# Optimization experiments

Measured on AMD Instinct MI355X. Metric: run time of the kernel, lower is better.

Reference implementation:

```python
import jax, jax.numpy as jnp
import numpy as np

SEQ, BATCH, D_MODEL, N_HEADS = 2048, 2, 1024, 16
HEAD_DIM = D_MODEL // N_HEADS


def setup_inputs() -> dict:
    key = jax.random.key(0)
    ks = jax.random.split(key, 5)
    scale = 1.0 / np.sqrt(D_MODEL)
    x = jax.random.normal(ks[0], (SEQ, BATCH, D_MODEL), dtype=jnp.float32)
    Wq = jax.random.normal(ks[1], (D_MODEL, D_MODEL), dtype=jnp.float32) * scale
    Wk = jax.random.normal(ks[2], (D_MODEL, D_MODEL), dtype=jnp.float32) * scale
    Wv = jax.random.normal(ks[3], (D_MODEL, D_MODEL), dtype=jnp.float32) * scale
    Wo = jax.random.normal(ks[4], (D_MODEL, D_MODEL), dtype=jnp.float32) * scale
    return {"x": x, "Wq": Wq, "Wk": Wk, "Wv": Wv, "Wo": Wo}


def reference(x, Wq, Wk, Wv, Wo):
    # x: (S, B, D). torch nn.Linear(bias=False): y = x @ W.T with W (out,in)
    S, B, D = x.shape
    H, Hd = N_HEADS, HEAD_DIM
    q = (x @ Wq.T).reshape(S, B, H, Hd)
    k = (x @ Wk.T).reshape(S, B, H, Hd)
    v = (x @ Wv.T).reshape(S, B, H, Hd)
    # scores: (B, H, S, S)
    scores = jnp.einsum("sbhd,tbhd->bhst", q, k) / jnp.sqrt(jnp.float32(Hd))
    causal = jnp.triu(jnp.ones((S, S), dtype=bool), k=1)  # True above diagonal
    scores = jnp.where(causal[None, None, :, :], -jnp.inf, scores)
    probs = jax.nn.softmax(scores, axis=-1)
    # out: (S, B, H, Hd) -> (S, B, D)
    attn = jnp.einsum("bhst,tbhd->sbhd", probs, v).reshape(S, B, D)
    return attn @ Wo.T
```

## Files before the change

### kernel.cpp

```cpp
#include <hip/hip_runtime.h>
#include <math.h>

#define SEQ     2048
#define BATCH   2
#define DMODEL  1024
#define NHEADS  16
#define HDIM    64
#define MROWS   (SEQ * BATCH)
#define KDIM    1024

typedef _Float16 half8  __attribute__((ext_vector_type(8)));
typedef _Float16 half2v __attribute__((ext_vector_type(2)));
typedef float    f32x4  __attribute__((ext_vector_type(4)));

__device__ inline void gload_lds16(const void* g, void* lds_uniform) {
    __builtin_amdgcn_global_load_lds(
        (const __attribute__((address_space(1))) void*)g,
        (__attribute__((address_space(3))) void*)lds_uniform,
        16, 0, 0);
}

__global__ __launch_bounds__(256)
void cvt_f32_f16(const float* __restrict__ s, _Float16* __restrict__ d, int n8) {
    const int i = blockIdx.x * 256 + threadIdx.x;
    if (i < n8) {
        const float4* sp = reinterpret_cast<const float4*>(s) + (size_t)i * 2;
        const float4 x0 = sp[0], x1 = sp[1];
        const half8 h = {(_Float16)x0.x, (_Float16)x0.y, (_Float16)x0.z, (_Float16)x0.w,
                         (_Float16)x1.x, (_Float16)x1.y, (_Float16)x1.z, (_Float16)x1.w};
        *(reinterpret_cast<half8*>(d) + i) = h;
    }
}

#define GBM 128
#define GBN 64

template<int AMODE, int QKV>
__global__ __launch_bounds__(256)
void gemm_k(const void* __restrict__ Ap, const _Float16* __restrict__ Wall,
            void* __restrict__ C0, void* __restrict__ C1, void* __restrict__ C2)
{
    __shared__ _Float16 As[2][GBM * 32];
    __shared__ _Float16 Bs[2][GBN * 32];

    const int tid  = threadIdx.x;
    const int wid  = tid >> 6;
    const int lane = tid & 63;
    const int m0 = blockIdx.y * GBM;
    const int n0 = blockIdx.x * GBN;
    const int wr = (wid >> 1) * 64;
    const int wc = (wid & 1) * 32;

    const _Float16* Wh = QKV ? (Wall + (size_t)blockIdx.z * KDIM * DMODEL) : Wall;

    const int a_row = tid >> 2;
    const int a_col = (tid & 3) * 8;
    const int b_row = wid * 16 + (lane >> 2);
    const int b_col = (lane & 3) * 8;

    const float*    Af0 = (const float*)Ap    + (size_t)(m0 + a_row)      * KDIM + a_col;
    const float*    Af1 = (const float*)Ap    + (size_t)(m0 + a_row + 64) * KDIM + a_col;
    const _Float16* Ah0 = (const _Float16*)Ap + (size_t)(m0 + a_row)      * KDIM + a_col;
    const _Float16* Ah1 = (const _Float16*)Ap + (size_t)(m0 + a_row + 64) * KDIM + a_col;
    const _Float16* Wr  = Wh + (size_t)(n0 + b_row) * KDIM + b_col;

    const int frow = lane & 15;
    const int kb   = (lane >> 4) * 8;

    f32x4 acc[4][2] = {};

    for (int k0 = 0; k0 < KDIM; k0 += 64) {
        #pragma unroll
        for (int s = 0; s < 2; ++s) {
            const int kk = k0 + s * 32;
            gload_lds16(Wr + kk, (char*)Bs[s] + wid * 1024);
            if constexpr (AMODE == 0) {
                const float4 a0 = *reinterpret_cast<const float4*>(Af0 + kk);
                const float4 a1 = *reinterpret_cast<const float4*>(Af0 + kk + 4);
                const float4 a2 = *reinterpret_cast<const float4*>(Af1 + kk);
                const float4 a3 = *reinterpret_cast<const float4*>(Af1 + kk + 4);
                const half8 h0 = {(_Float16)a0.x, (_Float16)a0.y, (_Float16)a0.z, (_Float16)a0.w,
                                  (_Float16)a1.x, (_Float16)a1.y, (_Float16)a1.z, (_Float16)a1.w};
                const half8 h1 = {(_Float16)a2.x, (_Float16)a2.y, (_Float16)a2.z, (_Float16)a2.w,
                                  (_Float16)a3.x, (_Float16)a3.y, (_Float16)a3.z, (_Float16)a3.w};
                *reinterpret_cast<half8*>((char*)As[s] + tid * 16)        = h0;
                *reinterpret_cast<half8*>((char*)As[s] + 4096 + tid * 16) = h1;
            } else {
                *reinterpret_cast<half8*>((char*)As[s] + tid * 16) =
                    *reinterpret_cast<const half8*>(Ah0 + kk);
                *reinterpret_cast<half8*>((char*)As[s] + 4096 + tid * 16) =
                    *reinterpret_cast<const half8*>(Ah1 + kk);
            }
        }
        __syncthreads();

        #pragma unroll
        for (int s = 0; s < 2; ++s) {
            half8 af[4], bf[2];
            #pragma unroll
            for (int fm = 0; fm < 4; ++fm)
                af[fm] = *reinterpret_cast<const half8*>(&As[s][(wr + fm * 16 + frow) * 32 + kb]);
            #pragma unroll
            for (int fn = 0; fn < 2; ++fn)
                bf[fn] = *reinterpret_cast<const half8*>(&Bs[s][(wc + fn * 16 + frow) * 32 + kb]);
            #pragma unroll
            for (int fm = 0; fm < 4; ++fm)
                #pragma unroll
                for (int fn = 0; fn < 2; ++fn)
                    acc[fm][fn] = __builtin_amdgcn_mfma_f32_16x16x32_f16(
                        af[fm], bf[fn], acc[fm][fn], 0, 0, 0);
        }
        __syncthreads();
    }

    const int crow = (lane >> 4) * 4;
    const int ccol = lane & 15;
    if constexpr (QKV == 0) {
        float* C = (float*)C0;
        #pragma unroll
        for (int fm = 0; fm < 4; ++fm)
            #pragma unroll
            for (int fn = 0; fn < 2; ++fn)
                #pragma unroll
                for (int r = 0; r < 4; ++r)
                    C[(size_t)(m0 + wr + fm * 16 + crow + r) * DMODEL
                      + n0 + wc + fn * 16 + ccol] = acc[fm][fn][r];
    } else {
        if (blockIdx.z < 2) {
            _Float16* C = (_Float16*)(blockIdx.z == 0 ? C0 : C1);
            #pragma unroll
            for (int fm = 0; fm < 4; ++fm)
                #pragma unroll
                for (int fn = 0; fn < 2; ++fn)
                    #pragma unroll
                    for (int r = 0; r < 4; ++r)
                        C[(size_t)(m0 + wr + fm * 16 + crow + r) * DMODEL
                          + n0 + wc + fn * 16 + ccol] = (_Float16)acc[fm][fn][r];
        } else {
            _Float16* Vt = (_Float16*)C2;
            const int hh = blockIdx.x;
            #pragma unroll
            for (int fm = 0; fm < 4; ++fm)
                #pragma unroll
                for (int fn = 0; fn < 2; ++fn) {
                    const int d  = wc + fn * 16 + ccol;
                    const int s0 = (m0 + wr + fm * 16 + crow) >> 1;
                    const half2v lo = {(_Float16)acc[fm][fn][0], (_Float16)acc[fm][fn][2]};
                    const half2v hi = {(_Float16)acc[fm][fn][1], (_Float16)acc[fm][fn][3]};
                    *reinterpret_cast<half2v*>(Vt + ((size_t)(hh * 64 + d)) * SEQ + s0) = lo;
                    *reinterpret_cast<half2v*>(Vt + ((size_t)((16 + hh) * 64 + d)) * SEQ + s0) = hi;
                }
        }
    }
}

__global__ __launch_bounds__(256)
void attn_mfma(const _Float16* __restrict__ Qh, const _Float16* __restrict__ Kh,
               const _Float16* __restrict__ Vt, _Float16* __restrict__ Ab)
{
    __shared__ _Float16 Qs[64 * 64];
    __shared__ _Float16 Ks[64 * 64];
    __shared__ _Float16 Vs[64 * 64];
    __shared__ _Float16 Ps[4 * 16 * 72];

    const int tid  = threadIdx.x;
    const int wid  = tid >> 6;
    const int lane = tid & 63;
    const int l4 = lane & 15, lg = lane >> 4;
    const int bh = blockIdx.y, b = bh >> 4, h = bh & 15;

    for (int half = 0; half < 2; ++half) {
        const int qt = half ? (31 - (int)blockIdx.x) : (int)blockIdx.x;
        const int q0 = qt * 64;

        __syncthreads();
        #pragma unroll
        for (int i = 0; i < 2; ++i) {
            const int row = i * 32 + wid * 8 + (lane >> 3);
            const int c   = (lane & 7) ^ (row & 7);
            gload_lds16(Qh + ((size_t)((q0 + row) * 2 + b)) * DMODEL + h * 64 + c * 8,
                        (char*)Qs + i * 4096 + wid * 1024);
        }
        __syncthreads();

        half8 qf[2];
        {
            const int row = wid * 16 + l4;
            #pragma unroll
            for (int ks = 0; ks < 2; ++ks) {
                const int p = (ks * 4 + lg) ^ (row & 7);
                qf[ks] = *reinterpret_cast<const half8*>((char*)Qs + row * 128 + p * 16);
            }
        }

        float m_r[4], l_r[4];
        f32x4 o[4] = {};
        #pragma unroll
        for (int r = 0; r < 4; ++r) { m_r[r] = -1e30f; l_r[r] = 0.f; }

        _Float16* Pw = Ps + wid * 16 * 72;
        const int ktiles = qt + 1;

        for (int kt = 0; kt < ktiles; ++kt) {
            const int t0 = kt * 64;
            __syncthreads();
            #pragma unroll
            for (int i = 0; i < 2; ++i) {
                const int row = i * 32 + wid * 8 + (lane >> 3);
                const int c   = (lane & 7) ^ (row & 7);
                gload_lds16(Kh + ((size_t)((t0 + row) * 2 + b)) * DMODEL + h * 64 + c * 8,
                            (char*)Ks + i * 4096 + wid * 1024);
                gload_lds16(Vt + ((size_t)(bh * 64 + row)) * SEQ + t0 + c * 8,
                            (char*)Vs + i * 4096 + wid * 1024);
            }
            __syncthreads();

            f32x4 sacc[4] = {};
            #pragma unroll
            for (int ks = 0; ks < 2; ++ks)
                #pragma unroll
                for (int fn = 0; fn < 4; ++fn) {
                    const int row = fn * 16 + l4;
                    const int p   = (ks * 4 + lg) ^ (row & 7);
                    const half8 bf = *reinterpret_cast<const half8*>((char*)Ks + row * 128 + p * 16);
                    sacc[fn] = __builtin_amdgcn_mfma_f32_16x16x32_f16(qf[ks], bf, sacc[fn], 0, 0, 0);
                }

            const int qbase = q0 + wid * 16 + lg * 4;
            float sv[4][4];
            #pragma unroll
            for (int fn = 0; fn < 4; ++fn) {
                const int tg = t0 + fn * 16 + l4;
                #pragma unroll
                for (int r = 0; r < 4; ++r)
                    sv[fn][r] = (tg <= qbase + r) ? sacc[fn][r] * 0.125f : -1e30f;
            }
            #pragma unroll
            for (int r = 0; r < 4; ++r) {
                float rm = fmaxf(fmaxf(sv[0][r], sv[1][r]), fmaxf(sv[2][r], sv[3][r]));
                rm = fmaxf(rm, __shfl_xor(rm, 1));
                rm = fmaxf(rm, __shfl_xor(rm, 2));
                rm = fmaxf(rm, __shfl_xor(rm, 4));
                rm = fmaxf(rm, __shfl_xor(rm, 8));
                const float mnew  = fmaxf(m_r[r], rm);
                const float alpha = __expf(m_r[r] - mnew);
                m_r[r] = mnew;
                float rs = 0.f;
                #pragma unroll
                for (int fn = 0; fn < 4; ++fn) {
                    const float pv = __expf(sv[fn][r] - mnew);
                    sv[fn][r] = pv; rs += pv;
                }
                rs += __shfl_xor(rs, 1); rs += __shfl_xor(rs, 2);
                rs += __shfl_xor(rs, 4); rs += __shfl_xor(rs, 8);
                l_r[r] = l_r[r] * alpha + rs;
                #pragma unroll
                for (int fn = 0; fn < 4; ++fn) o[fn][r] *= alpha;
            }

            #pragma unroll
            for (int fn = 0; fn < 4; ++fn)
                #pragma unroll
                for (int r = 0; r < 4; ++r)
                    Pw[(lg * 4 + r) * 72 + fn * 16 + l4] = (_Float16)sv[fn][r];

            half8 pf[2];
            #pragma unroll
            for (int ks = 0; ks < 2; ++ks)
                pf[ks] = *reinterpret_cast<const half8*>((char*)Pw + l4 * 144 + ks * 64 + lg * 16);

            #pragma unroll
            for (int ks = 0; ks < 2; ++ks)
                #pragma unroll
                for (int fn = 0; fn < 4; ++fn) {
                    const int row = fn * 16 + l4;
                    const int p   = (ks * 4 + lg) ^ (row & 7);
                    const half8 vf = *reinterpret_cast<const half8*>((char*)Vs + row * 128 + p * 16);
                    o[fn] = __builtin_amdgcn_mfma_f32_16x16x32_f16(pf[ks], vf, o[fn], 0, 0, 0);
                }
        }

        #pragma unroll
        for (int r = 0; r < 4; ++r) {
            const float inv = 1.0f / l_r[r];
            const size_t mrow = (size_t)((q0 + wid * 16 + lg * 4 + r) * 2 + b);
            #pragma unroll
            for (int fn = 0; fn < 4; ++fn)
                Ab[mrow * DMODEL + h * 64 + fn * 16 + l4] = (_Float16)(o[fn][r] * inv);
        }
    }
}

extern "C" void kernel_launch(void* const* d_in, const int* in_sizes, int n_in,
                              void* d_out, int out_size, void* d_ws, size_t ws_size,
                              hipStream_t stream) {
    const float* x  = (const float*)d_in[0];
    const float* Wq = (const float*)d_in[1];
    const float* Wk = (const float*)d_in[2];
    const float* Wv = (const float*)d_in[3];
    const float* Wo = (const float*)d_in[4];
    float* out = (float*)d_out;

    const size_t NELEM = (size_t)MROWS * DMODEL;
    const size_t WELEM = (size_t)DMODEL * DMODEL;
    _Float16* Qh = (_Float16*)d_ws;
    _Float16* Kh = Qh + NELEM;
    _Float16* Vt = Kh + NELEM;
    _Float16* Ab = Vt + NELEM;
    _Float16* Wh = Ab + NELEM;

    const int wn8 = (int)(WELEM / 8);
    const int cvt_blocks = (wn8 + 255) / 256;
    cvt_f32_f16<<<cvt_blocks, 256, 0, stream>>>(Wq, Wh + 0 * WELEM, wn8);
    cvt_f32_f16<<<cvt_blocks, 256, 0, stream>>>(Wk, Wh + 1 * WELEM, wn8);
    cvt_f32_f16<<<cvt_blocks, 256, 0, stream>>>(Wv, Wh + 2 * WELEM, wn8);
    cvt_f32_f16<<<cvt_blocks, 256, 0, stream>>>(Wo, Wh + 3 * WELEM, wn8);

    const dim3 qkv_grid(DMODEL / GBN, MROWS / GBM, 3);
    gemm_k<0,1><<<qkv_grid, 256, 0, stream>>>(x, Wh, Qh, Kh, Vt);

    const dim3 agrid(SEQ / 128, BATCH * NHEADS);
    attn_mfma<<<agrid, 256, 0, stream>>>(Qh, Kh, Vt, Ab);

    const dim3 ogrid(DMODEL / GBN, MROWS / GBM);
    gemm_k<1,0><<<ogrid, 256, 0, stream>>>(Ab, Wh + 3 * WELEM, out, nullptr, nullptr);
}
```

Baseline: 251.7 us.

## Pre-convert x, batch weight casts, async-load GEMM tiles, double-buffer attention K/V

x is converted to fp16 up front so both GEMMs can stream A and B tiles directly into swizzled LDS with global_load_lds, and the QKV GEMM moves to 128x128 tiles. The four weight conversions are merged into one launch. The attention kernel double-buffers its K/V tiles so the next tile's loads overlap the current tile's MFMA work, with one barrier per iteration instead of two. The cost is an extra conversion pass over x and more LDS and registers per block.

```diff
diff --git a/kernel.cpp b/kernel.cpp
--- a/kernel.cpp
+++ b/kernel.cpp
@@ -20,107 +20,100 @@
         16, 0, 0);
 }
 
+__device__ inline void cvt8(const float* sp, _Float16* dp) {
+    const float4 x0 = reinterpret_cast<const float4*>(sp)[0];
+    const float4 x1 = reinterpret_cast<const float4*>(sp)[1];
+    const half8 h = {(_Float16)x0.x, (_Float16)x0.y, (_Float16)x0.z, (_Float16)x0.w,
+                     (_Float16)x1.x, (_Float16)x1.y, (_Float16)x1.z, (_Float16)x1.w};
+    *reinterpret_cast<half8*>(dp) = h;
+}
+
 __global__ __launch_bounds__(256)
 void cvt_f32_f16(const float* __restrict__ s, _Float16* __restrict__ d, int n8) {
     const int i = blockIdx.x * 256 + threadIdx.x;
-    if (i < n8) {
-        const float4* sp = reinterpret_cast<const float4*>(s) + (size_t)i * 2;
-        const float4 x0 = sp[0], x1 = sp[1];
-        const half8 h = {(_Float16)x0.x, (_Float16)x0.y, (_Float16)x0.z, (_Float16)x0.w,
-                         (_Float16)x1.x, (_Float16)x1.y, (_Float16)x1.z, (_Float16)x1.w};
-        *(reinterpret_cast<half8*>(d) + i) = h;
-    }
-}
-
-#define GBM 128
-#define GBN 64
-
-template<int AMODE, int QKV>
+    if (i < n8) cvt8(s + (size_t)i * 8, d + (size_t)i * 8);
+}
+
 __global__ __launch_bounds__(256)
-void gemm_k(const void* __restrict__ Ap, const _Float16* __restrict__ Wall,
-            void* __restrict__ C0, void* __restrict__ C1, void* __restrict__ C2)
+void cvt4_w(const float* __restrict__ s0, const float* __restrict__ s1,
+            const float* __restrict__ s2, const float* __restrict__ s3,
+            _Float16* __restrict__ d) {
+    const int wsel = blockIdx.x >> 9;
+    const int i    = (blockIdx.x & 511) * 256 + threadIdx.x;
+    const float* s = (wsel == 0) ? s0 : (wsel == 1) ? s1 : (wsel == 2) ? s2 : s3;
+    cvt8(s + (size_t)i * 8, d + (size_t)wsel * DMODEL * KDIM + (size_t)i * 8);
+}
+
+template<int TBN, int EPI>
+__global__ __launch_bounds__(256)
+void gemm2(const _Float16* __restrict__ Ah, const _Float16* __restrict__ Wall,
+           void* __restrict__ C0, void* __restrict__ C1, void* __restrict__ C2)
 {
-    __shared__ _Float16 As[2][GBM * 32];
-    __shared__ _Float16 Bs[2][GBN * 32];
-
-    const int tid  = threadIdx.x;
-    const int wid  = tid >> 6;
-    const int lane = tid & 63;
-    const int m0 = blockIdx.y * GBM;
-    const int n0 = blockIdx.x * GBN;
-    const int wr = (wid >> 1) * 64;
-    const int wc = (wid & 1) * 32;
-
-    const _Float16* Wh = QKV ? (Wall + (size_t)blockIdx.z * KDIM * DMODEL) : Wall;
-
-    const int a_row = tid >> 2;
-    const int a_col = (tid & 3) * 8;
-    const int b_row = wid * 16 + (lane >> 2);
-    const int b_col = (lane & 3) * 8;
-
-    const float*    Af0 = (const float*)Ap    + (size_t)(m0 + a_row)      * KDIM + a_col;
-    const float*    Af1 = (const float*)Ap    + (size_t)(m0 + a_row + 64) * KDIM + a_col;
-    const _Float16* Ah0 = (const _Float16*)Ap + (size_t)(m0 + a_row)      * KDIM + a_col;
-    const _Float16* Ah1 = (const _Float16*)Ap + (size_t)(m0 + a_row + 64) * KDIM + a_col;
-    const _Float16* Wr  = Wh + (size_t)(n0 + b_row) * KDIM + b_col;
-
-    const int frow = lane & 15;
-    const int kb   = (lane >> 4) * 8;
-
-    f32x4 acc[4][2] = {};
+    constexpr int FN    = TBN / 32;
+    constexpr int B_ISS = TBN / 32;
+    __shared__ _Float16 As[128 * 64];
+    __shared__ _Float16 Bs[TBN * 64];
+
+    const int tid = threadIdx.x, wid = tid >> 6, lane = tid & 63;
+    const int m0 = blockIdx.y * 128, n0 = blockIdx.x * TBN;
+    const int wr = (wid >> 1) * 64, wc = (wid & 1) * (TBN / 2);
+    const _Float16* Wh = EPI ? (Wall + (size_t)blockIdx.z * KDIM * DMODEL) : Wall;
+
+    const int srow = wid * 8 + (lane >> 3);
+    const int sj   = lane & 7;
+    const int l4 = lane & 15, lg = lane >> 4;
+
+    f32x4 acc[4][FN] = {};
 
     for (int k0 = 0; k0 < KDIM; k0 += 64) {
         #pragma unroll
-        for (int s = 0; s < 2; ++s) {
-            const int kk = k0 + s * 32;
-            gload_lds16(Wr + kk, (char*)Bs[s] + wid * 1024);
-            if constexpr (AMODE == 0) {
-                const float4 a0 = *reinterpret_cast<const float4*>(Af0 + kk);
-                const float4 a1 = *reinterpret_cast<const float4*>(Af0 + kk + 4);
-                const float4 a2 = *reinterpret_cast<const float4*>(Af1 + kk);
-                const float4 a3 = *reinterpret_cast<const float4*>(Af1 + kk + 4);
-                const half8 h0 = {(_Float16)a0.x, (_Float16)a0.y, (_Float16)a0.z, (_Float16)a0.w,
-                                  (_Float16)a1.x, (_Float16)a1.y, (_Float16)a1.z, (_Float16)a1.w};
-                const half8 h1 = {(_Float16)a2.x, (_Float16)a2.y, (_Float16)a2.z, (_Float16)a2.w,
-                                  (_Float16)a3.x, (_Float16)a3.y, (_Float16)a3.z, (_Float16)a3.w};
-                *reinterpret_cast<half8*>((char*)As[s] + tid * 16)        = h0;
-                *reinterpret_cast<half8*>((char*)As[s] + 4096 + tid * 16) = h1;
-            } else {
-                *reinterpret_cast<half8*>((char*)As[s] + tid * 16) =
-                    *reinterpret_cast<const half8*>(Ah0 + kk);
-                *reinterpret_cast<half8*>((char*)As[s] + 4096 + tid * 16) =
-                    *reinterpret_cast<const half8*>(Ah1 + kk);
-            }
+        for (int i = 0; i < 4; ++i) {
+            const int row = i * 32 + srow;
+            const int c   = sj ^ (row & 7);
+            gload_lds16(Ah + (size_t)(m0 + row) * KDIM + k0 + c * 8,
+                        (char*)As + i * 4096 + wid * 1024);
+        }
+        #pragma unroll
+        for (int i = 0; i < B_ISS; ++i) {
+            const int row = i * 32 + srow;
+            const int c   = sj ^ (row & 7);
+            gload_lds16(Wh + (size_t)(n0 + row) * KDIM + k0 + c * 8,
+                        (char*)Bs + i * 4096 + wid * 1024);
         }
         __syncthreads();
 
         #pragma unroll
-        for (int s = 0; s < 2; ++s) {
-            half8 af[4], bf[2];
+        for (int ks = 0; ks < 2; ++ks) {
+            half8 af[4], bf[FN];
+            #pragma unroll
+            for (int fm = 0; fm < 4; ++fm) {
+                const int row = wr + fm * 16 + l4;
+                const int p   = (ks * 4 + lg) ^ (row & 7);
+                af[fm] = *reinterpret_cast<const half8*>((char*)As + row * 128 + p * 16);
+            }
+            #pragma unroll
+            for (int fn = 0; fn < FN; ++fn) {
+                const int row = wc + fn * 16 + l4;
+                const int p   = (ks * 4 + lg) ^ (row & 7);
+                bf[fn] = *reinterpret_cast<const half8*>((char*)Bs + row * 128 + p * 16);
+            }
             #pragma unroll
             for (int fm = 0; fm < 4; ++fm)
-                af[fm] = *reinterpret_cast<const half8*>(&As[s][(wr + fm * 16 + frow) * 32 + kb]);
-            #pragma unroll
-            for (int fn = 0; fn < 2; ++fn)
-                bf[fn] = *reinterpret_cast<const half8*>(&Bs[s][(wc + fn * 16 + frow) * 32 + kb]);
-            #pragma unroll
-            for (int fm = 0; fm < 4; ++fm)
-                #pragma unroll
-                for (int fn = 0; fn < 2; ++fn)
+                #pragma unroll
+                for (int fn = 0; fn < FN; ++fn)
                     acc[fm][fn] = __builtin_amdgcn_mfma_f32_16x16x32_f16(
                         af[fm], bf[fn], acc[fm][fn], 0, 0, 0);
         }
         __syncthreads();
     }
 
-    const int crow = (lane >> 4) * 4;
-    const int ccol = lane & 15;
-    if constexpr (QKV == 0) {
+    const int crow = lg * 4, ccol = l4;
+    if constexpr (EPI == 0) {
         float* C = (float*)C0;
         #pragma unroll
         for (int fm = 0; fm < 4; ++fm)
             #pragma unroll
-            for (int fn = 0; fn < 2; ++fn)
+            for (int fn = 0; fn < FN; ++fn)
                 #pragma unroll
                 for (int r = 0; r < 4; ++r)
                     C[(size_t)(m0 + wr + fm * 16 + crow + r) * DMODEL
@@ -131,19 +124,19 @@
             #pragma unroll
             for (int fm = 0; fm < 4; ++fm)
                 #pragma unroll
-                for (int fn = 0; fn < 2; ++fn)
+                for (int fn = 0; fn < FN; ++fn)
                     #pragma unroll
                     for (int r = 0; r < 4; ++r)
                         C[(size_t)(m0 + wr + fm * 16 + crow + r) * DMODEL
                           + n0 + wc + fn * 16 + ccol] = (_Float16)acc[fm][fn][r];
         } else {
             _Float16* Vt = (_Float16*)C2;
-            const int hh = blockIdx.x;
             #pragma unroll
             for (int fm = 0; fm < 4; ++fm)
                 #pragma unroll
-                for (int fn = 0; fn < 2; ++fn) {
-                    const int d  = wc + fn * 16 + ccol;
+                for (int fn = 0; fn < FN; ++fn) {
+                    const int ng = n0 + wc + fn * 16 + ccol;
+                    const int hh = ng >> 6, d = ng & 63;
                     const int s0 = (m0 + wr + fm * 16 + crow) >> 1;
                     const half2v lo = {(_Float16)acc[fm][fn][0], (_Float16)acc[fm][fn][2]};
                     const half2v hi = {(_Float16)acc[fm][fn][1], (_Float16)acc[fm][fn][3]};
@@ -154,13 +147,28 @@
     }
 }
 
+__device__ inline void stage_kv(const _Float16* __restrict__ Kh,
+                                const _Float16* __restrict__ Vt,
+                                _Float16* KsBuf, _Float16* VsBuf,
+                                int t0, int b, int bh, int h, int wid, int lane) {
+    #pragma unroll
+    for (int i = 0; i < 2; ++i) {
+        const int row = i * 32 + wid * 8 + (lane >> 3);
+        const int c   = (lane & 7) ^ (row & 7);
+        gload_lds16(Kh + ((size_t)((t0 + row) * 2 + b)) * DMODEL + h * 64 + c * 8,
+                    (char*)KsBuf + i * 4096 + wid * 1024);
+        gload_lds16(Vt + ((size_t)(bh * 64 + row)) * SEQ + t0 + c * 8,
+                    (char*)VsBuf + i * 4096 + wid * 1024);
+    }
+}
+
 __global__ __launch_bounds__(256)
 void attn_mfma(const _Float16* __restrict__ Qh, const _Float16* __restrict__ Kh,
                const _Float16* __restrict__ Vt, _Float16* __restrict__ Ab)
 {
     __shared__ _Float16 Qs[64 * 64];
-    __shared__ _Float16 Ks[64 * 64];
-    __shared__ _Float16 Vs[64 * 64];
+    __shared__ _Float16 Ks[2][64 * 64];
+    __shared__ _Float16 Vs[2][64 * 64];
     __shared__ _Float16 Ps[4 * 16 * 72];
 
     const int tid  = threadIdx.x;
@@ -172,6 +180,7 @@
     for (int half = 0; half < 2; ++half) {
         const int qt = half ? (31 - (int)blockIdx.x) : (int)blockIdx.x;
         const int q0 = qt * 64;
+        const int ktiles = qt + 1;
 
         __syncthreads();
         #pragma unroll
@@ -181,6 +190,7 @@
             gload_lds16(Qh + ((size_t)((q0 + row) * 2 + b)) * DMODEL + h * 64 + c * 8,
                         (char*)Qs + i * 4096 + wid * 1024);
         }
+        stage_kv(Kh, Vt, Ks[0], Vs[0], 0, b, bh, h, wid, lane);
         __syncthreads();
 
         half8 qf[2];
@@ -199,21 +209,13 @@
         for (int r = 0; r < 4; ++r) { m_r[r] = -1e30f; l_r[r] = 0.f; }
 
         _Float16* Pw = Ps + wid * 16 * 72;
-        const int ktiles = qt + 1;
 
         for (int kt = 0; kt < ktiles; ++kt) {
-            const int t0 = kt * 64;
-            __syncthreads();
-            #pragma unroll
-            for (int i = 0; i < 2; ++i) {
-                const int row = i * 32 + wid * 8 + (lane >> 3);
-                const int c   = (lane & 7) ^ (row & 7);
-                gload_lds16(Kh + ((size_t)((t0 + row) * 2 + b)) * DMODEL + h * 64 + c * 8,
-                            (char*)Ks + i * 4096 + wid * 1024);
-                gload_lds16(Vt + ((size_t)(bh * 64 + row)) * SEQ + t0 + c * 8,
-                            (char*)Vs + i * 4096 + wid * 1024);
-            }
-            __syncthreads();
+            const int t0  = kt * 64;
+            const int cur = kt & 1;
+
+            if (kt + 1 < ktiles)
+                stage_kv(Kh, Vt, Ks[cur ^ 1], Vs[cur ^ 1], t0 + 64, b, bh, h, wid, lane);
 
             f32x4 sacc[4] = {};
             #pragma unroll
@@ -222,7 +224,8 @@
                 for (int fn = 0; fn < 4; ++fn) {
                     const int row = fn * 16 + l4;
                     const int p   = (ks * 4 + lg) ^ (row & 7);
-                    const half8 bf = *reinterpret_cast<const half8*>((char*)Ks + row * 128 + p * 16);
+                    const half8 bf = *reinterpret_cast<const half8*>(
+                        (char*)Ks[cur] + row * 128 + p * 16);
                     sacc[fn] = __builtin_amdgcn_mfma_f32_16x16x32_f16(qf[ks], bf, sacc[fn], 0, 0, 0);
                 }
 
@@ -275,9 +278,14 @@
                 for (int fn = 0; fn < 4; ++fn) {
                     const int row = fn * 16 + l4;
                     const int p   = (ks * 4 + lg) ^ (row & 7);
-                    const half8 vf = *reinterpret_cast<const half8*>((char*)Vs + row * 128 + p * 16);
+                    const half8 vf = *reinterpret_cast<const half8*>(
+                        (char*)Vs[cur] + row * 128 + p * 16);
                     o[fn] = __builtin_amdgcn_mfma_f32_16x16x32_f16(pf[ks], vf, o[fn], 0, 0, 0);
                 }
+
+            asm volatile("s_waitcnt vmcnt(0)" ::: "memory");
+            __builtin_amdgcn_s_barrier();
+            __builtin_amdgcn_sched_barrier(0);
         }
 
         #pragma unroll
@@ -303,25 +311,21 @@
 
     const size_t NELEM = (size_t)MROWS * DMODEL;
     const size_t WELEM = (size_t)DMODEL * DMODEL;
-    _Float16* Qh = (_Float16*)d_ws;
-    _Float16* Kh = Qh + NELEM;
-    _Float16* Vt = Kh + NELEM;
-    _Float16* Ab = Vt + NELEM;
-    _Float16* Wh = Ab + NELEM;
-
-    const int wn8 = (int)(WELEM / 8);
-    const int cvt_blocks = (wn8 + 255) / 256;
-    cvt_f32_f16<<<cvt_blocks, 256, 0, stream>>>(Wq, Wh + 0 * WELEM, wn8);
-    cvt_f32_f16<<<cvt_blocks, 256, 0, stream>>>(Wk, Wh + 1 * WELEM, wn8);
-    cvt_f32_f16<<<cvt_blocks, 256, 0, stream>>>(Wv, Wh + 2 * WELEM, wn8);
-    cvt_f32_f16<<<cvt_blocks, 256, 0, stream>>>(Wo, Wh + 3 * WELEM, wn8);
-
-    const dim3 qkv_grid(DMODEL / GBN, MROWS / GBM, 3);
-    gemm_k<0,1><<<qkv_grid, 256, 0, stream>>>(x, Wh, Qh, Kh, Vt);
+    _Float16* Qh   = (_Float16*)d_ws;
+    _Float16* Kh   = Qh + NELEM;
+    _Float16* Vt   = Kh + NELEM;
+    _Float16* AbXh = Vt + NELEM;
+    _Float16* Wh   = AbXh + NELEM;
+
+    cvt_f32_f16<<<(int)(NELEM / 8 / 256), 256, 0, stream>>>(x, AbXh, (int)(NELEM / 8));
+    cvt4_w<<<2048, 256, 0, stream>>>(Wq, Wk, Wv, Wo, Wh);
+
+    const dim3 qkv_grid(DMODEL / 128, MROWS / 128, 3);
+    gemm2<128, 1><<<qkv_grid, 256, 0, stream>>>(AbXh, Wh, Qh, Kh, Vt);
 
     const dim3 agrid(SEQ / 128, BATCH * NHEADS);
-    attn_mfma<<<agrid, 256, 0, stream>>>(Qh, Kh, Vt, Ab);
-
-    const dim3 ogrid(DMODEL / GBN, MROWS / GBM);
-    gemm_k<1,0><<<ogrid, 256, 0, stream>>>(Ab, Wh + 3 * WELEM, out, nullptr, nullptr);
-}
+    attn_mfma<<<agrid, 256, 0, stream>>>(Qh, Kh, Vt, AbXh);
+
+    const dim3 ogrid(DMODEL / 64, MROWS / 128);
+    gemm2<64, 0><<<ogrid, 256, 0, stream>>>(AbXh, Wh + 3 * WELEM, out, nullptr, nullptr);
+}
```

Result: faster. 218.4 us (-13.2%).
